# Optimization experiments

Measured on AMD Instinct MI355X. Metric: run time of the kernel, lower is better.

The kernel has to match this reference:

```python
import jax, jax.numpy as jnp
import numpy as np

B, S, V, E, H = 2048, 128, 128, 300, 512  # batch, max_length, vocab, embed, hidden (enc_outstate_dim == H)


def setup_inputs() -> dict:
    key = jax.random.key(0)
    ks = jax.random.split(key, 20)
    s = 0.05
    return {
        "x": jax.random.randint(ks[0], (B, 1), 0, V),
        "hidden": jax.random.normal(ks[1], (1, B, H), jnp.float32),
        "enc_output": jax.random.normal(ks[2], (B, S, H), jnp.float32),
        "emb_table": jax.random.normal(ks[3], (V, E), jnp.float32) * s,
        "W1_w": jax.random.normal(ks[4], (H, H), jnp.float32) * s,
        "W1_b": jnp.zeros((H,), jnp.float32),
        "W2_w": jax.random.normal(ks[5], (H, H), jnp.float32) * s,
        "W2_b": jnp.zeros((H,), jnp.float32),
        "V_w": jax.random.normal(ks[6], (1, H), jnp.float32) * s,
        "V_b": jnp.zeros((1,), jnp.float32),
        "gru_w_ih": jax.random.normal(ks[7], (3 * H, E + H), jnp.float32) * s,
        "gru_w_hh": jax.random.normal(ks[8], (3 * H, H), jnp.float32) * s,
        "gru_b_ih": jnp.zeros((3 * H,), jnp.float32),
        "gru_b_hh": jnp.zeros((3 * H,), jnp.float32),
        "fc1_w": jax.random.normal(ks[9], (E, H), jnp.float32) * s,
        "fc1_b": jnp.zeros((E,), jnp.float32),
        "fc2_w": jax.random.normal(ks[10], (V, E), jnp.float32) * s,
        "fc2_b": jnp.zeros((V,), jnp.float32),
    }


def reference(x, hidden, enc_output, emb_table, W1_w, W1_b, W2_w, W2_b, V_w, V_b,
              gru_w_ih, gru_w_hh, gru_b_ih, gru_b_hh, fc1_w, fc1_b, fc2_w, fc2_b):
    emb = emb_table[x[:, 0]]  # [B,E]
    # Bahdanau additive attention
    hsum = jnp.sum(hidden, axis=0)  # [B,H] (sum over layers)
    score = jnp.tanh(enc_output @ W1_w.T + W1_b + (hsum @ W2_w.T + W2_b)[:, None, :])  # [B,S,H]
    attw = jax.nn.softmax(score @ V_w.T + V_b, axis=1)  # [B,S,1]
    ctx = jnp.sum(attw * enc_output, axis=1)  # [B,H]
    # single-step GRU (PyTorch gate layout: r,z,n)
    gin = jnp.concatenate([ctx, emb], axis=-1)  # [B,H+E]
    h0 = hidden[0]
    gi = gin @ gru_w_ih.T + gru_b_ih
    gh = h0 @ gru_w_hh.T + gru_b_hh
    i_r, i_z, i_n = gi[:, :H], gi[:, H:2 * H], gi[:, 2 * H:]
    h_r, h_z, h_n = gh[:, :H], gh[:, H:2 * H], gh[:, 2 * H:]
    r = jax.nn.sigmoid(i_r + h_r)
    z = jax.nn.sigmoid(i_z + h_z)
    n = jnp.tanh(i_n + r * h_n)
    h_new = (1.0 - z) * n + z * h0  # [B,H]
    # FC head
    y = jax.nn.leaky_relu(h_new @ fc1_w.T + fc1_b, 0.01) @ fc2_w.T + fc2_b  # [B,V]
    return y, h_new[None]
```

## Files before the change

### kernel.cpp

```cpp
#include <hip/hip_runtime.h>


typedef __attribute__((ext_vector_type(4))) float floatx4;
typedef __attribute__((ext_vector_type(8))) short short8;

#define DEV static __device__ __forceinline__

DEV unsigned short f2bf(float f) {
  unsigned u = __float_as_uint(f);
  u = u + 0x7fffu + ((u >> 16) & 1u);
  return (unsigned short)(u >> 16);
}
DEV float bf2f(unsigned short s) { return __uint_as_float(((unsigned)s) << 16); }
DEV float tanh_fast(float x) {
  float e = __expf(2.f * x);
  return 1.f - 2.f / (e + 1.f);
}
DEV float sigmoid_fast(float x) { return 1.f / (1.f + __expf(-x)); }

DEV void convpad_body(const float* __restrict__ src,
                      unsigned short* __restrict__ dst,
                      int idx, int Nsrc, int Kin, int Kp) {
  int n = idx / Kp, k = idx - n * Kp;
  float v = (k < Kin && n < Nsrc) ? src[(size_t)n * Kin + k] : 0.f;
  dst[idx] = f2bf(v);
}

#define PB_W1 1024
#define PB_W2 1024
#define PB_WIH 4992
#define PB_WHH 3072
#define PB_FC1 768
#define PB_FC2 192
#define PB_HID 4096
#define PB_EMB 2560
#define PB_BIAS 2
#define PREP_BLOCKS (PB_W1 + PB_W2 + PB_WIH + PB_WHH + PB_FC1 + PB_FC2 + PB_HID + PB_EMB + PB_BIAS)

__global__ void prep_all(
    const float* __restrict__ W1w, unsigned short* __restrict__ W1bf,
    const float* __restrict__ W2w, unsigned short* __restrict__ W2bf,
    const float* __restrict__ wih, unsigned short* __restrict__ wihbf,
    const float* __restrict__ whh, unsigned short* __restrict__ whhbf,
    const float* __restrict__ fc1w, unsigned short* __restrict__ fc1wbf,
    const float* __restrict__ fc2w, unsigned short* __restrict__ fc2wbf,
    const float* __restrict__ hidden, unsigned short* __restrict__ hidbf,
    const int* __restrict__ x, const float* __restrict__ embt,
    unsigned short* __restrict__ gin,
    const float* __restrict__ W1b, const float* __restrict__ W2b,
    float* __restrict__ keyb,
    const float* __restrict__ fc1b, float* __restrict__ fc1bp) {
  int bid = blockIdx.x;
  int tid = threadIdx.x;
  if (bid < PB_W1) {
    convpad_body(W1w, W1bf, bid * 256 + tid, 512, 512, 512);
    return;
  }
  bid -= PB_W1;
  if (bid < PB_W2) {
    convpad_body(W2w, W2bf, bid * 256 + tid, 512, 512, 512);
    return;
  }
  bid -= PB_W2;
  if (bid < PB_WIH) {
    convpad_body(wih, wihbf, bid * 256 + tid, 1536, 812, 832);
    return;
  }
  bid -= PB_WIH;
  if (bid < PB_WHH) {
    convpad_body(whh, whhbf, bid * 256 + tid, 1536, 512, 512);
    return;
  }
  bid -= PB_WHH;
  if (bid < PB_FC1) {
    convpad_body(fc1w, fc1wbf, bid * 256 + tid, 300, 512, 512);
    return;
  }
  bid -= PB_FC1;
  if (bid < PB_FC2) {
    convpad_body(fc2w, fc2wbf, bid * 256 + tid, 128, 300, 384);
    return;
  }
  bid -= PB_FC2;
  if (bid < PB_HID) {
    convpad_body(hidden, hidbf, bid * 256 + tid, 2048, 512, 512);
    return;
  }
  bid -= PB_HID;
  if (bid < PB_EMB) {
    int idx = bid * 256 + tid;
    int b = idx / 320, e = idx - b * 320;
    float v = (e < 300) ? embt[(size_t)x[b] * 300 + e] : 0.f;
    gin[(size_t)b * 832 + 512 + e] = f2bf(v);
    return;
  }
  bid -= PB_EMB;
  {
    int i = bid * 256 + tid;
    if (i < 512) keyb[i] = W1b[i] + W2b[i];
    if (i < 384) fc1bp[i] = (i < 300) ? fc1b[i] : 0.f;
  }
}

template <int EPI>
__global__ __launch_bounds__(256, 3) void gemm_bt(
    const unsigned short* __restrict__ A, int lda,
    const unsigned short* __restrict__ Bm, int ldb,
    const float* __restrict__ bias,
    void* __restrict__ Cp, int ldc, int K) {
  __shared__ unsigned short As[128 * 64];
  __shared__ unsigned short Bs[128 * 64];
  int tid = threadIdx.x;
  int bm = blockIdx.x * 128, bn = blockIdx.y * 128;
  int lane = tid & 63, wave = tid >> 6;
  int l15 = lane & 15, l4 = lane >> 4;
  int wm = (wave >> 1) * 64, wn = (wave & 1) * 64;

  floatx4 zero = {0.f, 0.f, 0.f, 0.f};
  floatx4 acc[4][4];
#pragma unroll
  for (int i = 0; i < 4; ++i)
#pragma unroll
    for (int j = 0; j < 4; ++j) acc[i][j] = zero;

  int row = tid >> 1;
  int gc0 = (tid & 1) * 4;
  const unsigned short* Aptr = A + (size_t)(bm + row) * lda + gc0 * 8;
  const unsigned short* Bptr = Bm + (size_t)(bn + row) * ldb + gc0 * 8;
  int rslot7 = row & 7, lslot7 = l15 & 7;

  int nk = K >> 6;
  for (int kt = 0; kt < nk; ++kt) {
#pragma unroll
    for (int i = 0; i < 4; ++i) {
      int slot = (gc0 + i) ^ rslot7;
      *(uint4*)&As[row * 64 + slot * 8] = *(const uint4*)(Aptr + kt * 64 + i * 8);
      *(uint4*)&Bs[row * 64 + slot * 8] = *(const uint4*)(Bptr + kt * 64 + i * 8);
    }
    __syncthreads();
#pragma unroll
    for (int ks = 0; ks < 2; ++ks) {
      int slot = (ks * 4 + l4) ^ lslot7;
      short8 av[4], bv[4];
#pragma unroll
      for (int mt = 0; mt < 4; ++mt)
        av[mt] = *(const short8*)&As[(wm + mt * 16 + l15) * 64 + slot * 8];
#pragma unroll
      for (int nt = 0; nt < 4; ++nt)
        bv[nt] = *(const short8*)&Bs[(wn + nt * 16 + l15) * 64 + slot * 8];
#pragma unroll
      for (int mt = 0; mt < 4; ++mt)
#pragma unroll
        for (int nt = 0; nt < 4; ++nt)
          acc[mt][nt] = __builtin_amdgcn_mfma_f32_16x16x32_bf16(
              av[mt], bv[nt], acc[mt][nt], 0, 0, 0);
    }
    __syncthreads();
  }

#pragma unroll
  for (int nt = 0; nt < 4; ++nt) {
    int n = bn + wn + nt * 16 + l15;
    float bvv = bias[n];
#pragma unroll
    for (int mt = 0; mt < 4; ++mt) {
#pragma unroll
      for (int r = 0; r < 4; ++r) {
        int m = bm + wm + mt * 16 + l4 * 4 + r;
        float v = acc[mt][nt][r] + bvv;
        if (EPI == 1) {
          v = v > 0.f ? v : 0.01f * v;
          ((unsigned short*)Cp)[(size_t)m * ldc + n] = f2bf(v);
        } else {
          ((float*)Cp)[(size_t)m * ldc + n] = v;
        }
      }
    }
  }
}

#define ATTN_LDS_BYTES (128 * 512 * 2 + 8 * 128 * 4 + 128 * 4)

__global__ __launch_bounds__(512, 2) void attn_kernel(
    const float* __restrict__ enc, const unsigned short* __restrict__ W1b16,
    const float* __restrict__ key, const float* __restrict__ Vw,
    unsigned short* __restrict__ gin) {
  extern __shared__ unsigned char smem_raw[];
  unsigned short* Albs = (unsigned short*)smem_raw;
  float* lds_part = (float*)(smem_raw + 128 * 512 * 2);
  float* lds_attw = lds_part + 8 * 128;

  int b = blockIdx.x;
  int tid = threadIdx.x;
  const float* encb = enc + (size_t)b * 128 * 512;

#pragma unroll 2
  for (int it = 0; it < 16; ++it) {
    int g = it * 512 + tid;
    int m = g >> 6, gc = g & 63;
    const float4* src = (const float4*)(encb + (size_t)g * 8);
    float4 lo = src[0], hi = src[1];
    uint4 pk;
    pk.x = (unsigned)f2bf(lo.x) | ((unsigned)f2bf(lo.y) << 16);
    pk.y = (unsigned)f2bf(lo.z) | ((unsigned)f2bf(lo.w) << 16);
    pk.z = (unsigned)f2bf(hi.x) | ((unsigned)f2bf(hi.y) << 16);
    pk.w = (unsigned)f2bf(hi.z) | ((unsigned)f2bf(hi.w) << 16);
    int slot = gc ^ (m & 7);
    *(uint4*)&Albs[m * 512 + slot * 8] = pk;
  }
  __syncthreads();

  int wave = tid >> 6, lane = tid & 63;
  int l15 = lane & 15, l4 = lane >> 4, lslot7 = l15 & 7;
  int n0 = wave * 64;

  floatx4 zero = {0.f, 0.f, 0.f, 0.f};
  floatx4 acc[8][4];
#pragma unroll
  for (int i = 0; i < 8; ++i)
#pragma unroll
    for (int j = 0; j < 4; ++j) acc[i][j] = zero;

#pragma unroll 2
  for (int kt = 0; kt < 16; ++kt) {
    int slot = (kt * 4 + l4) ^ lslot7;
    short8 av[8], bv[4];
#pragma unroll
    for (int nt = 0; nt < 4; ++nt) {
      int n = n0 + nt * 16 + l15;
      bv[nt] = *(const short8*)(W1b16 + (size_t)n * 512 + kt * 32 + l4 * 8);
    }
#pragma unroll
    for (int mt = 0; mt < 8; ++mt)
      av[mt] = *(const short8*)&Albs[(mt * 16 + l15) * 512 + slot * 8];
#pragma unroll
    for (int mt = 0; mt < 8; ++mt)
#pragma unroll
      for (int nt = 0; nt < 4; ++nt)
        acc[mt][nt] = __builtin_amdgcn_mfma_f32_16x16x32_bf16(
            av[mt], bv[nt], acc[mt][nt], 0, 0, 0);
  }

  float kb[4], vwl[4];
#pragma unroll
  for (int nt = 0; nt < 4; ++nt) {
    int col = n0 + nt * 16 + l15;
    kb[nt] = key[(size_t)b * 512 + col];
    vwl[nt] = Vw[col];
  }
#pragma unroll
  for (int mt = 0; mt < 8; ++mt) {
#pragma unroll
    for (int r = 0; r < 4; ++r) {
      float c = 0.f;
#pragma unroll
      for (int nt = 0; nt < 4; ++nt)
        c += tanh_fast(acc[mt][nt][r] + kb[nt]) * vwl[nt];
      c += __shfl_xor(c, 1, 64);
      c += __shfl_xor(c, 2, 64);
      c += __shfl_xor(c, 4, 64);
      c += __shfl_xor(c, 8, 64);
      if (l15 == 0) lds_part[wave * 128 + mt * 16 + l4 * 4 + r] = c;
    }
  }
  __syncthreads();

  if (wave == 0) {
    float l0 = 0.f, l1 = 0.f;
#pragma unroll
    for (int w = 0; w < 8; ++w) {
      l0 += lds_part[w * 128 + lane];
      l1 += lds_part[w * 128 + lane + 64];
    }
    float mx = fmaxf(l0, l1);
#pragma unroll
    for (int o = 32; o >= 1; o >>= 1) mx = fmaxf(mx, __shfl_xor(mx, o, 64));
    float e0 = __expf(l0 - mx), e1 = __expf(l1 - mx);
    float s = e0 + e1;
#pragma unroll
    for (int o = 32; o >= 1; o >>= 1) s += __shfl_xor(s, o, 64);
    float inv = 1.f / s;
    lds_attw[lane] = e0 * inv;
    lds_attw[lane + 64] = e1 * inv;
  }
  __syncthreads();

  int h = tid, gc = h >> 3, off = h & 7;
  float cx = 0.f;
  for (int s = 0; s < 128; ++s)
    cx += lds_attw[s] * bf2f(Albs[s * 512 + ((gc ^ (s & 7)) << 3) + off]);
  gin[(size_t)b * 832 + h] = f2bf(cx);
}

__global__ void gru_kernel(const float* __restrict__ gi,
                           const float* __restrict__ gh,
                           const float* __restrict__ hidden,
                           float* __restrict__ outh,
                           unsigned short* __restrict__ hnewbf) {
  int idx = blockIdx.x * 256 + threadIdx.x;
  int b = idx >> 9, h = idx & 511;
  const float* gib = gi + (size_t)b * 1536;
  const float* ghb = gh + (size_t)b * 1536;
  float r = sigmoid_fast(gib[h] + ghb[h]);
  float z = sigmoid_fast(gib[512 + h] + ghb[512 + h]);
  float n = tanh_fast(gib[1024 + h] + r * ghb[1024 + h]);
  float h0 = hidden[idx];
  float hn = (1.f - z) * n + z * h0;
  outh[idx] = hn;
  hnewbf[idx] = f2bf(hn);
}

extern "C" void kernel_launch(void* const* d_in, const int* in_sizes, int n_in,
                              void* d_out, int out_size, void* d_ws,
                              size_t ws_size, hipStream_t stream) {
  const int* x = (const int*)d_in[0];
  const float* hidden = (const float*)d_in[1];
  const float* enc = (const float*)d_in[2];
  const float* embt = (const float*)d_in[3];
  const float* W1w = (const float*)d_in[4];
  const float* W1b = (const float*)d_in[5];
  const float* W2w = (const float*)d_in[6];
  const float* W2b = (const float*)d_in[7];
  const float* Vw = (const float*)d_in[8];
  const float* wih = (const float*)d_in[10];
  const float* whh = (const float*)d_in[11];
  const float* bih = (const float*)d_in[12];
  const float* bhh = (const float*)d_in[13];
  const float* fc1w = (const float*)d_in[14];
  const float* fc1b = (const float*)d_in[15];
  const float* fc2w = (const float*)d_in[16];
  const float* fc2b = (const float*)d_in[17];

  float* out_y = (float*)d_out;
  float* out_h = out_y + 2048 * 128;

  char* ws = (char*)d_ws;
  size_t o = 0;
  auto alloc = [&](size_t bytes) {
    size_t r = o;
    o += (bytes + 255) & ~(size_t)255;
    return r;
  };
  unsigned short* W1bf = (unsigned short*)(ws + alloc(512 * 512 * 2));
  unsigned short* W2bf = (unsigned short*)(ws + alloc(512 * 512 * 2));
  unsigned short* wihbf = (unsigned short*)(ws + alloc(1536 * 832 * 2));
  unsigned short* whhbf = (unsigned short*)(ws + alloc(1536 * 512 * 2));
  unsigned short* fc1wbf = (unsigned short*)(ws + alloc(384 * 512 * 2));
  unsigned short* fc2wbf = (unsigned short*)(ws + alloc(128 * 384 * 2));
  unsigned short* hidbf = (unsigned short*)(ws + alloc(2048 * 512 * 2));
  unsigned short* ginbf = (unsigned short*)(ws + alloc((size_t)2048 * 832 * 2));
  float* keyb = (float*)(ws + alloc(512 * 4));
  float* fc1bp = (float*)(ws + alloc(384 * 4));
  float* key = (float*)(ws + alloc((size_t)2048 * 512 * 4));
  float* gi = (float*)(ws + alloc((size_t)2048 * 1536 * 4));
  float* gh = (float*)(ws + alloc((size_t)2048 * 1536 * 4));
  unsigned short* hnewbf = (unsigned short*)(ws + alloc(2048 * 512 * 2));
  unsigned short* a1bf = (unsigned short*)(ws + alloc((size_t)2048 * 384 * 2));

  prep_all<<<PREP_BLOCKS, 256, 0, stream>>>(
      W1w, W1bf, W2w, W2bf, wih, wihbf, whh, whhbf, fc1w, fc1wbf, fc2w, fc2wbf,
      hidden, hidbf, x, embt, ginbf, W1b, W2b, keyb, fc1b, fc1bp);

  gemm_bt<0><<<dim3(16, 4), 256, 0, stream>>>(hidbf, 512, W2bf, 512, keyb,
                                              (void*)key, 512, 512);

  (void)hipFuncSetAttribute((const void*)attn_kernel,
                            hipFuncAttributeMaxDynamicSharedMemorySize,
                            ATTN_LDS_BYTES);
  attn_kernel<<<2048, 512, ATTN_LDS_BYTES, stream>>>(enc, W1bf, key, Vw, ginbf);

  gemm_bt<0><<<dim3(16, 12), 256, 0, stream>>>(hidbf, 512, whhbf, 512, bhh,
                                               (void*)gh, 1536, 512);
  gemm_bt<0><<<dim3(16, 12), 256, 0, stream>>>(ginbf, 832, wihbf, 832, bih,
                                               (void*)gi, 1536, 832);
  gru_kernel<<<2048 * 512 / 256, 256, 0, stream>>>(gi, gh, hidden, out_h, hnewbf);

  gemm_bt<1><<<dim3(16, 3), 256, 0, stream>>>(hnewbf, 512, fc1wbf, 512, fc1bp,
                                              (void*)a1bf, 384, 512);
  gemm_bt<0><<<dim3(16, 1), 256, 0, stream>>>(a1bf, 384, fc2wbf, 384, fc2b,
                                              (void*)out_y, 128, 384);
}
```

Before: 1.006 ms.

## Split attention into half-sequence logits kernel and separate softmax-context kernel

The fused attention kernel is split in two. The first kernel computes score logits for half of the sequence per block, using 64 KB of static LDS so more blocks can be resident per CU. The second kernel does the softmax and the weighted context sum by reading enc_output again from global memory in fp32. This trades one extra 2048x128x512 fp32 read of enc_output (about 0.5 GB) and an extra launch for higher occupancy and less per-block LDS; the context is now computed in fp32 rather than from bf16-rounded enc.

```diff
diff --git a/kernel.cpp b/kernel.cpp
--- a/kernel.cpp
+++ b/kernel.cpp
@@ -179,23 +179,19 @@
   }
 }
 
-#define ATTN_LDS_BYTES (128 * 512 * 2 + 8 * 128 * 4 + 128 * 4)
-
-__global__ __launch_bounds__(512, 2) void attn_kernel(
+__global__ __launch_bounds__(512, 4) void logits_kernel(
     const float* __restrict__ enc, const unsigned short* __restrict__ W1b16,
     const float* __restrict__ key, const float* __restrict__ Vw,
-    unsigned short* __restrict__ gin) {
-  extern __shared__ unsigned char smem_raw[];
-  unsigned short* Albs = (unsigned short*)smem_raw;
-  float* lds_part = (float*)(smem_raw + 128 * 512 * 2);
-  float* lds_attw = lds_part + 8 * 128;
-
-  int b = blockIdx.x;
+    float* __restrict__ logits) {
+  __shared__ unsigned short Albs[64 * 512];
+  float* lds_part = (float*)Albs;
+
+  int b = blockIdx.x, sh = blockIdx.y;
   int tid = threadIdx.x;
-  const float* encb = enc + (size_t)b * 128 * 512;
+  const float* encb = enc + ((size_t)b * 128 + (size_t)sh * 64) * 512;
 
 #pragma unroll 2
-  for (int it = 0; it < 16; ++it) {
+  for (int it = 0; it < 8; ++it) {
     int g = it * 512 + tid;
     int m = g >> 6, gc = g & 63;
     const float4* src = (const float4*)(encb + (size_t)g * 8);
@@ -215,26 +211,26 @@
   int n0 = wave * 64;
 
   floatx4 zero = {0.f, 0.f, 0.f, 0.f};
-  floatx4 acc[8][4];
-#pragma unroll
-  for (int i = 0; i < 8; ++i)
+  floatx4 acc[4][4];
+#pragma unroll
+  for (int i = 0; i < 4; ++i)
 #pragma unroll
     for (int j = 0; j < 4; ++j) acc[i][j] = zero;
 
 #pragma unroll 2
   for (int kt = 0; kt < 16; ++kt) {
     int slot = (kt * 4 + l4) ^ lslot7;
-    short8 av[8], bv[4];
+    short8 av[4], bv[4];
 #pragma unroll
     for (int nt = 0; nt < 4; ++nt) {
       int n = n0 + nt * 16 + l15;
       bv[nt] = *(const short8*)(W1b16 + (size_t)n * 512 + kt * 32 + l4 * 8);
     }
 #pragma unroll
-    for (int mt = 0; mt < 8; ++mt)
+    for (int mt = 0; mt < 4; ++mt)
       av[mt] = *(const short8*)&Albs[(mt * 16 + l15) * 512 + slot * 8];
 #pragma unroll
-    for (int mt = 0; mt < 8; ++mt)
+    for (int mt = 0; mt < 4; ++mt)
 #pragma unroll
       for (int nt = 0; nt < 4; ++nt)
         acc[mt][nt] = __builtin_amdgcn_mfma_f32_16x16x32_bf16(
@@ -248,8 +244,9 @@
     kb[nt] = key[(size_t)b * 512 + col];
     vwl[nt] = Vw[col];
   }
-#pragma unroll
-  for (int mt = 0; mt < 8; ++mt) {
+  float part[4][4];
+#pragma unroll
+  for (int mt = 0; mt < 4; ++mt) {
 #pragma unroll
     for (int r = 0; r < 4; ++r) {
       float c = 0.f;
@@ -260,18 +257,34 @@
       c += __shfl_xor(c, 2, 64);
       c += __shfl_xor(c, 4, 64);
       c += __shfl_xor(c, 8, 64);
-      if (l15 == 0) lds_part[wave * 128 + mt * 16 + l4 * 4 + r] = c;
+      part[mt][r] = c;
     }
   }
   __syncthreads();
+#pragma unroll
+  for (int mt = 0; mt < 4; ++mt)
+#pragma unroll
+    for (int r = 0; r < 4; ++r)
+      if (l15 == 0) lds_part[wave * 64 + mt * 16 + l4 * 4 + r] = part[mt][r];
+  __syncthreads();
 
   if (wave == 0) {
-    float l0 = 0.f, l1 = 0.f;
-#pragma unroll
-    for (int w = 0; w < 8; ++w) {
-      l0 += lds_part[w * 128 + lane];
-      l1 += lds_part[w * 128 + lane + 64];
-    }
+    float l = 0.f;
+#pragma unroll
+    for (int w = 0; w < 8; ++w) l += lds_part[w * 64 + lane];
+    logits[(size_t)b * 128 + sh * 64 + lane] = l;
+  }
+}
+
+__global__ __launch_bounds__(128, 8) void ctx_kernel(
+    const float* __restrict__ enc, const float* __restrict__ logits,
+    unsigned short* __restrict__ gin) {
+  __shared__ float attw[128];
+  int b = blockIdx.x, tid = threadIdx.x;
+
+  if (tid < 64) {
+    float l0 = logits[(size_t)b * 128 + tid];
+    float l1 = logits[(size_t)b * 128 + 64 + tid];
     float mx = fmaxf(l0, l1);
 #pragma unroll
     for (int o = 32; o >= 1; o >>= 1) mx = fmaxf(mx, __shfl_xor(mx, o, 64));
@@ -280,16 +293,28 @@
 #pragma unroll
     for (int o = 32; o >= 1; o >>= 1) s += __shfl_xor(s, o, 64);
     float inv = 1.f / s;
-    lds_attw[lane] = e0 * inv;
-    lds_attw[lane + 64] = e1 * inv;
+    attw[tid] = e0 * inv;
+    attw[tid + 64] = e1 * inv;
   }
   __syncthreads();
 
-  int h = tid, gc = h >> 3, off = h & 7;
-  float cx = 0.f;
-  for (int s = 0; s < 128; ++s)
-    cx += lds_attw[s] * bf2f(Albs[s * 512 + ((gc ^ (s & 7)) << 3) + off]);
-  gin[(size_t)b * 832 + h] = f2bf(cx);
+  const float* encb = enc + (size_t)b * 128 * 512;
+  float4 cx = {0.f, 0.f, 0.f, 0.f};
+#pragma unroll 4
+  for (int s = 0; s < 128; ++s) {
+    float w = attw[s];
+    float4 v = *(const float4*)(encb + (size_t)s * 512 + tid * 4);
+    cx.x += w * v.x;
+    cx.y += w * v.y;
+    cx.z += w * v.z;
+    cx.w += w * v.w;
+  }
+  ushort4 pk;
+  pk.x = f2bf(cx.x);
+  pk.y = f2bf(cx.y);
+  pk.z = f2bf(cx.z);
+  pk.w = f2bf(cx.w);
+  *(ushort4*)&gin[(size_t)b * 832 + tid * 4] = pk;
 }
 
 __global__ void gru_kernel(const float* __restrict__ gi,
@@ -352,6 +377,7 @@
   float* keyb = (float*)(ws + alloc(512 * 4));
   float* fc1bp = (float*)(ws + alloc(384 * 4));
   float* key = (float*)(ws + alloc((size_t)2048 * 512 * 4));
+  float* logits = (float*)(ws + alloc((size_t)2048 * 128 * 4));
   float* gi = (float*)(ws + alloc((size_t)2048 * 1536 * 4));
   float* gh = (float*)(ws + alloc((size_t)2048 * 1536 * 4));
   unsigned short* hnewbf = (unsigned short*)(ws + alloc(2048 * 512 * 2));
@@ -364,10 +390,8 @@
   gemm_bt<0><<<dim3(16, 4), 256, 0, stream>>>(hidbf, 512, W2bf, 512, keyb,
                                               (void*)key, 512, 512);
 
-  (void)hipFuncSetAttribute((const void*)attn_kernel,
-                            hipFuncAttributeMaxDynamicSharedMemorySize,
-                            ATTN_LDS_BYTES);
-  attn_kernel<<<2048, 512, ATTN_LDS_BYTES, stream>>>(enc, W1bf, key, Vw, ginbf);
+  logits_kernel<<<dim3(2048, 2), 512, 0, stream>>>(enc, W1bf, key, Vw, logits);
+  ctx_kernel<<<2048, 128, 0, stream>>>(enc, logits, ginbf);
 
   gemm_bt<0><<<dim3(16, 12), 256, 0, stream>>>(hidbf, 512, whhbf, 512, bhh,
                                                (void*)gh, 1536, 512);
```

New measurement: 1.095 ms. 1.09x slower.

## Stream enc_output directly from global in attention, drop LDS staging

Applied to the files above, without the earlier changes.

The attention kernel no longer converts each batch's 128x512 encoder tile to bf16 in LDS. Each wave now loads its fp32 A fragments straight from global memory and converts them in registers with packed bf16 conversion, and the context sum re-reads enc_output in fp32 and reduces per-wave partials through a small LDS buffer. This removes the 128KB LDS footprint and its staging barrier, allowing higher occupancy. In exchange, every wave re-reads the same A rows, which multiplies global/L2 traffic for enc_output, and the context is now computed from fp32 rather than bf16 values.

```diff
diff --git a/kernel.cpp b/kernel.cpp
--- a/kernel.cpp
+++ b/kernel.cpp
@@ -1,4 +1,5 @@
 #include <hip/hip_runtime.h>
+#include <hip/hip_bf16.h>
 
 
 typedef __attribute__((ext_vector_type(4))) float floatx4;
@@ -17,6 +18,25 @@
   return 1.f - 2.f / (e + 1.f);
 }
 DEV float sigmoid_fast(float x) { return 1.f / (1.f + __expf(-x)); }
+
+DEV unsigned pk2(float a, float b) {
+  float2 f;
+  f.x = a;
+  f.y = b;
+  __hip_bfloat162 h = __float22bfloat162_rn(f);
+  return *(unsigned*)&h;
+}
+DEV short8 cvt8(float4 lo, float4 hi) {
+  union {
+    unsigned u[4];
+    short8 s;
+  } r;
+  r.u[0] = pk2(lo.x, lo.y);
+  r.u[1] = pk2(lo.z, lo.w);
+  r.u[2] = pk2(hi.x, hi.y);
+  r.u[3] = pk2(hi.z, hi.w);
+  return r.s;
+}
 
 DEV void convpad_body(const float* __restrict__ src,
                       unsigned short* __restrict__ dst,
@@ -179,40 +199,20 @@
   }
 }
 
-#define ATTN_LDS_BYTES (128 * 512 * 2 + 8 * 128 * 4 + 128 * 4)
-
-__global__ __launch_bounds__(512, 2) void attn_kernel(
+__global__ __launch_bounds__(512, 2) void attn_fused(
     const float* __restrict__ enc, const unsigned short* __restrict__ W1b16,
     const float* __restrict__ key, const float* __restrict__ Vw,
     unsigned short* __restrict__ gin) {
-  extern __shared__ unsigned char smem_raw[];
-  unsigned short* Albs = (unsigned short*)smem_raw;
-  float* lds_part = (float*)(smem_raw + 128 * 512 * 2);
-  float* lds_attw = lds_part + 8 * 128;
+  __shared__ float lds_part[8 * 128];
+  __shared__ float attw[128];
+  __shared__ float ctxp[8 * 512];
 
   int b = blockIdx.x;
   int tid = threadIdx.x;
+  int wave = tid >> 6, lane = tid & 63;
+  int l15 = lane & 15, l4 = lane >> 4;
+  int n0 = wave * 64;
   const float* encb = enc + (size_t)b * 128 * 512;
-
-#pragma unroll 2
-  for (int it = 0; it < 16; ++it) {
-    int g = it * 512 + tid;
-    int m = g >> 6, gc = g & 63;
-    const float4* src = (const float4*)(encb + (size_t)g * 8);
-    float4 lo = src[0], hi = src[1];
-    uint4 pk;
-    pk.x = (unsigned)f2bf(lo.x) | ((unsigned)f2bf(lo.y) << 16);
-    pk.y = (unsigned)f2bf(lo.z) | ((unsigned)f2bf(lo.w) << 16);
-    pk.z = (unsigned)f2bf(hi.x) | ((unsigned)f2bf(hi.y) << 16);
-    pk.w = (unsigned)f2bf(hi.z) | ((unsigned)f2bf(hi.w) << 16);
-    int slot = gc ^ (m & 7);
-    *(uint4*)&Albs[m * 512 + slot * 8] = pk;
-  }
-  __syncthreads();
-
-  int wave = tid >> 6, lane = tid & 63;
-  int l15 = lane & 15, l4 = lane >> 4, lslot7 = l15 & 7;
-  int n0 = wave * 64;
 
   floatx4 zero = {0.f, 0.f, 0.f, 0.f};
   floatx4 acc[8][4];
@@ -221,24 +221,26 @@
 #pragma unroll
     for (int j = 0; j < 4; ++j) acc[i][j] = zero;
 
+  const float* abase = encb + (size_t)l15 * 512 + l4 * 8;
+  const unsigned short* bbase = W1b16 + (size_t)(n0 + l15) * 512 + l4 * 8;
+
 #pragma unroll 2
   for (int kt = 0; kt < 16; ++kt) {
-    int slot = (kt * 4 + l4) ^ lslot7;
-    short8 av[8], bv[4];
-#pragma unroll
-    for (int nt = 0; nt < 4; ++nt) {
-      int n = n0 + nt * 16 + l15;
-      bv[nt] = *(const short8*)(W1b16 + (size_t)n * 512 + kt * 32 + l4 * 8);
-    }
-#pragma unroll
-    for (int mt = 0; mt < 8; ++mt)
-      av[mt] = *(const short8*)&Albs[(mt * 16 + l15) * 512 + slot * 8];
-#pragma unroll
-    for (int mt = 0; mt < 8; ++mt)
+    short8 bv[4];
+#pragma unroll
+    for (int nt = 0; nt < 4; ++nt)
+      bv[nt] = *(const short8*)(bbase + (size_t)nt * 16 * 512 + kt * 32);
+#pragma unroll
+    for (int mt = 0; mt < 8; ++mt) {
+      const float* ap = abase + mt * 16 * 512 + kt * 32;
+      float4 lo = *(const float4*)ap;
+      float4 hi = *(const float4*)(ap + 4);
+      short8 av = cvt8(lo, hi);
 #pragma unroll
       for (int nt = 0; nt < 4; ++nt)
         acc[mt][nt] = __builtin_amdgcn_mfma_f32_16x16x32_bf16(
-            av[mt], bv[nt], acc[mt][nt], 0, 0, 0);
+            av, bv[nt], acc[mt][nt], 0, 0, 0);
+    }
   }
 
   float kb[4], vwl[4];
@@ -270,7 +272,7 @@
 #pragma unroll
     for (int w = 0; w < 8; ++w) {
       l0 += lds_part[w * 128 + lane];
-      l1 += lds_part[w * 128 + lane + 64];
+      l1 += lds_part[w * 128 + 64 + lane];
     }
     float mx = fmaxf(l0, l1);
 #pragma unroll
@@ -280,16 +282,40 @@
 #pragma unroll
     for (int o = 32; o >= 1; o >>= 1) s += __shfl_xor(s, o, 64);
     float inv = 1.f / s;
-    lds_attw[lane] = e0 * inv;
-    lds_attw[lane + 64] = e1 * inv;
+    attw[lane] = e0 * inv;
+    attw[lane + 64] = e1 * inv;
   }
   __syncthreads();
 
-  int h = tid, gc = h >> 3, off = h & 7;
-  float cx = 0.f;
-  for (int s = 0; s < 128; ++s)
-    cx += lds_attw[s] * bf2f(Albs[s * 512 + ((gc ^ (s & 7)) << 3) + off]);
-  gin[(size_t)b * 832 + h] = f2bf(cx);
+  {
+    float4 cx0 = {0.f, 0.f, 0.f, 0.f}, cx1 = {0.f, 0.f, 0.f, 0.f};
+    const float* ep = encb + (size_t)(wave * 16) * 512 + lane * 4;
+#pragma unroll 4
+    for (int i = 0; i < 16; ++i) {
+      float w = attw[wave * 16 + i];
+      float4 v0 = *(const float4*)(ep + (size_t)i * 512);
+      float4 v1 = *(const float4*)(ep + (size_t)i * 512 + 256);
+      cx0.x += w * v0.x;
+      cx0.y += w * v0.y;
+      cx0.z += w * v0.z;
+      cx0.w += w * v0.w;
+      cx1.x += w * v1.x;
+      cx1.y += w * v1.y;
+      cx1.z += w * v1.z;
+      cx1.w += w * v1.w;
+    }
+    *(float4*)&ctxp[wave * 512 + lane * 4] = cx0;
+    *(float4*)&ctxp[wave * 512 + 256 + lane * 4] = cx1;
+  }
+  __syncthreads();
+
+  {
+    int h = tid;
+    float s = 0.f;
+#pragma unroll
+    for (int w = 0; w < 8; ++w) s += ctxp[w * 512 + h];
+    gin[(size_t)b * 832 + h] = f2bf(s);
+  }
 }
 
 __global__ void gru_kernel(const float* __restrict__ gi,
@@ -364,10 +390,7 @@
   gemm_bt<0><<<dim3(16, 4), 256, 0, stream>>>(hidbf, 512, W2bf, 512, keyb,
                                               (void*)key, 512, 512);
 
-  (void)hipFuncSetAttribute((const void*)attn_kernel,
-                            hipFuncAttributeMaxDynamicSharedMemorySize,
-                            ATTN_LDS_BYTES);
-  attn_kernel<<<2048, 512, ATTN_LDS_BYTES, stream>>>(enc, W1bf, key, Vw, ginbf);
+  attn_fused<<<2048, 512, 0, stream>>>(enc, W1bf, key, Vw, ginbf);
 
   gemm_bt<0><<<dim3(16, 12), 256, 0, stream>>>(hidbf, 512, whhbf, 512, bhh,
                                                (void*)gh, 1536, 512);
```

After: 1.673 ms. +66.2%, slower.
